# Optimization experiments

Measured on AMD Instinct MI355X. Metric: run time of the kernel, lower is better.

Reference implementation:

```python
import jax, jax.numpy as jnp
import numpy as np

B, S, D = 1, 1024, 2048          # batch, seq, hidden
H, KH, HD = 16, 16, 128          # heads, kv heads, head_dim
E, K, FI = 8, 4, 1408            # experts, top_k, moe_intermediate
FS = 5632                        # shared expert intermediate
WIN = 512                        # sliding window
THETA = 1.0e6                    # rope base
EPS = 1e-6                       # rmsnorm eps


def setup_inputs() -> dict:
    key = jax.random.key(0)
    ks = jax.random.split(key, 16)
    nrm = lambda k, shape: jax.random.normal(k, shape, jnp.float32) * 0.02
    return dict(
        hidden_states=jax.random.normal(ks[0], (B, S, D), jnp.float32),
        ln1_w=jnp.ones((D,), jnp.float32),
        ln2_w=jnp.ones((D,), jnp.float32),
        wq=nrm(ks[1], (D, H * HD)), bq=jnp.zeros((H * HD,), jnp.float32),
        wk=nrm(ks[2], (D, KH * HD)), bk=jnp.zeros((KH * HD,), jnp.float32),
        wv=nrm(ks[3], (D, KH * HD)), bv=jnp.zeros((KH * HD,), jnp.float32),
        wo=nrm(ks[4], (H * HD, D)),
        w_router=nrm(ks[5], (D, E)),
        w_gate_e=nrm(ks[6], (E, D, FI)),
        w_up_e=nrm(ks[7], (E, D, FI)),
        w_down_e=nrm(ks[8], (E, FI, D)),
        ws_gate=nrm(ks[9], (D, FS)),
        ws_up=nrm(ks[10], (D, FS)),
        ws_down=nrm(ks[11], (FS, D)),
        w_shared_gate=nrm(ks[12], (D, 1)),
    )


def _rms(h, w):
    v = jnp.mean(h * h, axis=-1, keepdims=True)
    return h * jax.lax.rsqrt(v + EPS) * w


def _rope(q, k):
    pos = jnp.arange(S, dtype=jnp.float32)
    inv = 1.0 / (THETA ** (jnp.arange(0, HD, 2, dtype=jnp.float32) / HD))
    ang = pos[:, None] * inv[None, :]                      # [S, HD/2]
    cos = jnp.concatenate([jnp.cos(ang)] * 2, -1)[None, :, None, :]
    sin = jnp.concatenate([jnp.sin(ang)] * 2, -1)[None, :, None, :]
    rot = lambda t: jnp.concatenate([-t[..., HD // 2:], t[..., :HD // 2]], -1)
    return q * cos + rot(q) * sin, k * cos + rot(k) * sin


def reference(hidden_states, ln1_w, ln2_w, wq, bq, wk, bk, wv, bv, wo,
              w_router, w_gate_e, w_up_e, w_down_e,
              ws_gate, ws_up, ws_down, w_shared_gate):
    x = hidden_states
    # --- sliding-window causal attention ---
    h = _rms(x, ln1_w)
    q = (h @ wq + bq).reshape(B, S, H, HD)
    k = (h @ wk + bk).reshape(B, S, KH, HD)
    v = (h @ wv + bv).reshape(B, S, KH, HD)
    q, k = _rope(q, k)
    scores = jnp.einsum('bqhd,bkhd->bhqk', q, k) * (HD ** -0.5)
    i = jnp.arange(S)[:, None]
    j = jnp.arange(S)[None, :]
    mask = (j <= i) & (i - j < WIN)                        # causal + window
    scores = jnp.where(mask[None, None], scores, jnp.finfo(scores.dtype).min)
    attn = jax.nn.softmax(scores, axis=-1)
    o = jnp.einsum('bhqk,bkhd->bqhd', attn, v).reshape(B, S, H * HD) @ wo
    x = x + o
    # --- sparse MoE block ---
    h = _rms(x, ln2_w)
    t = h.reshape(B * S, D)
    logits = (t @ w_router).astype(jnp.float32)
    probs = jax.nn.softmax(logits, axis=-1)                # [T, E]
    top_w, top_i = jax.lax.top_k(probs, K)                 # norm_topk_prob=False
    cw = jnp.zeros((B * S, E), probs.dtype).at[jnp.arange(B * S)[:, None], top_i].set(top_w)
    # routed experts (dense combine == gather/dispatch/grouped-GEMM/combine)
    g = jnp.einsum('td,edf->etf', t, w_gate_e)
    u = jnp.einsum('td,edf->etf', t, w_up_e)
    eo = jnp.einsum('etf,efd->etd', jax.nn.silu(g) * u, w_down_e)
    routed = jnp.einsum('te,etd->td', cw, eo)
    # shared expert with sigmoid gate
    shared = (jax.nn.silu(t @ ws_gate) * (t @ ws_up)) @ ws_down
    sgate = jax.nn.sigmoid(t @ w_shared_gate)              # [T, 1]
    moe = routed + sgate * shared
    return x + moe.reshape(B, S, D)
```

## Files before the change

### kernel.cpp

```cpp
#include <hip/hip_runtime.h>

#define S_ 1024
#define D_ 2048
#define H_ 16
#define HD_ 128
#define E_ 8
#define FI_ 1408
#define FS_ 5632
#define WIN_ 512
#define T_ 1024
#define QKVN 6144

typedef _Float16 f16;
typedef __attribute__((ext_vector_type(8))) _Float16 f16x8;
typedef __attribute__((ext_vector_type(4))) _Float16 f16x4;
typedef __attribute__((ext_vector_type(4))) float f32x4;

#define MFMA16(a, b, c) __builtin_amdgcn_mfma_f32_16x16x32_f16((a), (b), (c), 0, 0, 0)

__device__ __forceinline__ void gload16(const void* g, void* l) {
    __builtin_amdgcn_global_load_lds(
        (const __attribute__((address_space(1))) unsigned*)g,
        (__attribute__((address_space(3))) unsigned*)l, 16, 0, 0);
}

__global__ __launch_bounds__(256) void rmsnorm16_kernel(const float* __restrict__ x,
                                                        const float* __restrict__ w,
                                                        f16* __restrict__ out) {
    int t = blockIdx.x;
    const float* xr = x + (long)t * D_;
    int base = threadIdx.x * 8;
    float4 v0 = *(const float4*)(xr + base);
    float4 v1 = *(const float4*)(xr + base + 4);
    float ss = v0.x*v0.x + v0.y*v0.y + v0.z*v0.z + v0.w*v0.w
             + v1.x*v1.x + v1.y*v1.y + v1.z*v1.z + v1.w*v1.w;
    #pragma unroll
    for (int off = 1; off < 64; off <<= 1) ss += __shfl_xor(ss, off);
    __shared__ float red[4];
    if ((threadIdx.x & 63) == 0) red[threadIdx.x >> 6] = ss;
    __syncthreads();
    float tot = red[0] + red[1] + red[2] + red[3];
    float scale = rsqrtf(tot / (float)D_ + 1e-6f);
    float4 w0 = *(const float4*)(w + base);
    float4 w1 = *(const float4*)(w + base + 4);
    f16x8 o;
    o[0] = (f16)(v0.x*scale*w0.x); o[1] = (f16)(v0.y*scale*w0.y);
    o[2] = (f16)(v0.z*scale*w0.z); o[3] = (f16)(v0.w*scale*w0.w);
    o[4] = (f16)(v1.x*scale*w1.x); o[5] = (f16)(v1.y*scale*w1.y);
    o[6] = (f16)(v1.z*scale*w1.z); o[7] = (f16)(v1.w*scale*w1.w);
    *(f16x8*)(out + (long)t * D_ + base) = o;
}

__device__ __forceinline__ void tconv_body(const float* __restrict__ src,
                                           f16* __restrict__ dst,
                                           int K, int N, int mode) {
    int n0 = blockIdx.x * 64, k0 = blockIdx.y * 64;
    __shared__ f16 tile[64][72];
    int t = threadIdx.x, r = t >> 2, c4 = (t & 3) * 16;
    const float* sp = src + (long)(k0 + r) * N + n0 + c4;
    #pragma unroll
    for (int i = 0; i < 16; i += 4) {
        float4 v = *(const float4*)(sp + i);
        tile[c4 + i + 0][r] = (f16)v.x;
        tile[c4 + i + 1][r] = (f16)v.y;
        tile[c4 + i + 2][r] = (f16)v.z;
        tile[c4 + i + 3][r] = (f16)v.w;
    }
    __syncthreads();
    #pragma unroll
    for (int h = 0; h < 2; h++) {
        int v = t + h * 256;
        int nl = v >> 3, c8 = (v & 7) * 8;
        f16x8 vec = *(const f16x8*)&tile[nl][c8];
        int nr = n0 + nl;
        long orow = (mode == 0) ? nr
                  : ((long)(nr >> 4) * 32 + (nr & 15) + (mode == 2 ? 16 : 0));
        *(f16x8*)(dst + orow * K + k0 + c8) = vec;
    }
}

__global__ __launch_bounds__(256) void tconv_kernel(const float* __restrict__ src,
                                                    f16* __restrict__ dst,
                                                    int K, int N, long sSrc, long sDst) {
    tconv_body(src + (long)blockIdx.z * sSrc, dst + (long)blockIdx.z * sDst, K, N, 0);
}

__global__ __launch_bounds__(256) void tconv_gu_kernel(const float* __restrict__ srcA,
                                                       const float* __restrict__ srcB,
                                                       f16* __restrict__ dst,
                                                       int K, int N, long sSrc, long sDst,
                                                       int zsplit) {
    int z = blockIdx.z;
    int e = (z < zsplit) ? z : z - zsplit;
    const float* src = ((z < zsplit) ? srcA : srcB) + (long)e * sSrc;
    tconv_body(src, dst + (long)e * sDst, K, N, (z < zsplit) ? 1 : 2);
}

template <int EPI, int MODE>
__global__ __launch_bounds__(256) void gemm16_kernel(
    const f16* __restrict__ Ag, const f16* __restrict__ BTg,
    void* Cg, const void* auxg,
    const int* __restrict__ tokidx, const int* __restrict__ cntv,
    const float* __restrict__ tw,
    int M, int N, int K, int lda, int ldb,
    long sA, long sB, long sC) {
    int z = blockIdx.z;
    const f16* A = Ag + (long)z * sA;
    const f16* BT = BTg + (long)z * sB;
    int bm = blockIdx.y * 128, bn = blockIdx.x * 128;
    int cnt = M;
    if (MODE >= 1) {
        cnt = cntv[z];
        if (bm >= cnt) return;
    }
    int tid = threadIdx.x, lane = tid & 63, wave = tid >> 6;
    int wm = (wave >> 1) * 64, wn = (wave & 1) * 64;

    __shared__ f16 As[128][64];
    __shared__ f16 Bs[128][64];

    f32x4 acc[4][4];
    #pragma unroll
    for (int i = 0; i < 4; i++)
        #pragma unroll
        for (int j = 0; j < 4; j++) acc[i][j] = (f32x4){0.f, 0.f, 0.f, 0.f};

    int srow8 = lane >> 3;
    int scol = ((lane & 7) ^ srow8) * 8;
    const f16* Abp[4];
    const f16* Bbp[4];
    #pragma unroll
    for (int i = 0; i < 4; i++) {
        int ra = bm + wave * 32 + i * 8 + srow8;
        long arow;
        if (MODE == 1) {
            int tok = (ra < cnt) ? tokidx[z * T_ + ra] : 0;
            arow = tok;
        } else {
            arow = ra;
        }
        Abp[i] = A + arow * (long)lda + scol;
        Bbp[i] = BT + (long)(bn + wave * 32 + i * 8 + srow8) * ldb + scol;
    }

    for (int k0 = 0; k0 < K; k0 += 64) {
        __syncthreads();
        #pragma unroll
        for (int i = 0; i < 4; i++) {
            gload16(Abp[i] + k0, &As[wave * 32 + i * 8][0]);
            gload16(Bbp[i] + k0, &Bs[wave * 32 + i * 8][0]);
        }
        __syncthreads();
        #pragma unroll
        for (int kk = 0; kk < 64; kk += 32) {
            f16x8 af[4], bf[4];
            #pragma unroll
            for (int mi = 0; mi < 4; mi++) {
                int r = wm + mi * 16 + (lane & 15);
                int c = ((kk >> 3) + (lane >> 4)) ^ (r & 7);
                af[mi] = *(const f16x8*)((const char*)&As[r][0] + (c << 4));
            }
            #pragma unroll
            for (int ni = 0; ni < 4; ni++) {
                int r = wn + ni * 16 + (lane & 15);
                int c = ((kk >> 3) + (lane >> 4)) ^ (r & 7);
                bf[ni] = *(const f16x8*)((const char*)&Bs[r][0] + (c << 4));
            }
            #pragma unroll
            for (int mi = 0; mi < 4; mi++)
                #pragma unroll
                for (int ni = 0; ni < 4; ni++)
                    acc[mi][ni] = MFMA16(af[mi], bf[ni], acc[mi][ni]);
        }
    }

    if (EPI == 5) {
        int half = N >> 1;
        #pragma unroll
        for (int mi = 0; mi < 4; mi++) {
            #pragma unroll
            for (int p = 0; p < 2; p++) {
                #pragma unroll
                for (int i = 0; i < 4; i++) {
                    int m = bm + wm + mi * 16 + (lane >> 4) * 4 + i;
                    int j = ((bn + wn) >> 1) + p * 16 + (lane & 15);
                    float g = acc[mi][2 * p][i];
                    float u = acc[mi][2 * p + 1][i];
                    ((f16*)Cg + (long)z * sC)[(long)m * half + j] =
                        (f16)(g / (1.f + __expf(-g)) * u);
                }
            }
        }
        return;
    }
    #pragma unroll
    for (int mi = 0; mi < 4; mi++) {
        #pragma unroll
        for (int ni = 0; ni < 4; ni++) {
            #pragma unroll
            for (int i = 0; i < 4; i++) {
                int m = bm + wm + mi * 16 + (lane >> 4) * 4 + i;
                int n = bn + wn + ni * 16 + (lane & 15);
                long idx = (long)m * N + n;
                float v = acc[mi][ni][i];
                if (EPI == 1) {
                    ((f16*)Cg)[idx] = (f16)(v + ((const float*)auxg)[n]);
                } else if (EPI == 4) {
                    ((float*)Cg + (long)z * sC)[idx] = v;
                } else if (EPI == 6) {
                    float wv = tw[z * T_ + m];
                    ((f16*)Cg + (long)z * sC)[idx] = (f16)(v * wv);
                }
            }
        }
    }
}

__global__ __launch_bounds__(256) void rope16_kernel(f16* __restrict__ qkv) {
    int s = blockIdx.x;
    float fs = (float)s;
    for (int p = threadIdx.x; p < H_ * 64; p += 256) {
        int h = p >> 6, j = p & 63;
        float inv = __expf(-(float)j * (13.815510557964274f / 64.f));
        float ang = fs * inv;
        float c = cosf(ang), sn = sinf(ang);
        long base = (long)s * QKVN + h * HD_ + j;
        float q1 = (float)qkv[base], q2 = (float)qkv[base + 64];
        qkv[base] = (f16)(q1 * c - q2 * sn);
        qkv[base + 64] = (f16)(q2 * c + q1 * sn);
        long kb = base + 2048;
        float k1 = (float)qkv[kb], k2 = (float)qkv[kb + 64];
        qkv[kb] = (f16)(k1 * c - k2 * sn);
        qkv[kb + 64] = (f16)(k2 * c + k1 * sn);
    }
}

__global__ __launch_bounds__(256) void attn16_kernel(const f16* __restrict__ qkv,
                                                     f16* __restrict__ Og) {
    int qt = blockIdx.x * 64;
    int head = blockIdx.y;
    int tid = threadIdx.x, lane = tid & 63, wave = tid >> 6;

    __shared__ f16 Ks[64][128];
    __shared__ f16 Vrow[64][128];
    __shared__ f16 VsT[128][64];
    __shared__ f16 Ps[4][16][64];

    int qr = qt + wave * 16 + (lane & 15);
    const f16* Qp = qkv + (long)qr * QKVN + head * HD_;
    f16x8 qf[4];
    #pragma unroll
    for (int kk = 0; kk < 4; kk++)
        qf[kk] = *(const f16x8*)(Qp + kk * 32 + (lane >> 4) * 8);

    f32x4 oacc[8];
    #pragma unroll
    for (int db = 0; db < 8; db++) oacc[db] = (f32x4){0.f, 0.f, 0.f, 0.f};
    float m_run[4] = {-1e30f, -1e30f, -1e30f, -1e30f};
    float l_run[4] = {0.f, 0.f, 0.f, 0.f};

    int k_lo = qt - (WIN_ - 1);
    if (k_lo < 0) k_lo = 0;
    k_lo &= ~63;

    for (int k0 = k_lo; k0 < qt + 64; k0 += 64) {
        __syncthreads();
        {
            int row = tid >> 2, cq = (tid & 3) * 32;
            const f16* Kp = qkv + (long)(k0 + row) * QKVN + 2048 + head * HD_ + cq;
            const f16* Vp = Kp + 2048;
            #pragma unroll
            for (int u = 0; u < 32; u += 8) {
                f16x8 tk = *(const f16x8*)(Kp + u);
                int co = ((cq + u) * 2) ^ ((row & 7) << 4);
                *(f16x8*)((char*)&Ks[row][0] + co) = tk;
                *(f16x8*)(&Vrow[row][cq + u]) = *(const f16x8*)(Vp + u);
            }
        }
        __syncthreads();
        {
            int d = tid >> 1, ks = (tid & 1) * 32;
            f16 tmp[32];
            #pragma unroll
            for (int j = 0; j < 32; j++) tmp[j] = Vrow[ks + j][d];
            #pragma unroll
            for (int u = 0; u < 32; u += 8) {
                int co = ((ks + u) * 2) ^ ((d & 7) << 4);
                f16x8 tv;
                #pragma unroll
                for (int j = 0; j < 8; j++) tv[j] = tmp[u + j];
                *(f16x8*)((char*)&VsT[d][0] + co) = tv;
            }
        }
        f32x4 sacc[4];
        #pragma unroll
        for (int cb = 0; cb < 4; cb++) sacc[cb] = (f32x4){0.f, 0.f, 0.f, 0.f};
        #pragma unroll
        for (int kk = 0; kk < 4; kk++) {
            #pragma unroll
            for (int cb = 0; cb < 4; cb++) {
                int krow = cb * 16 + (lane & 15);
                int co = ((kk * 32 + (lane >> 4) * 8) * 2) ^ ((krow & 7) << 4);
                f16x8 kf = *(const f16x8*)((const char*)&Ks[krow][0] + co);
                sacc[cb] = MFMA16(qf[kk], kf, sacc[cb]);
            }
        }
        float mtile[4] = {-1e30f, -1e30f, -1e30f, -1e30f};
        #pragma unroll
        for (int cb = 0; cb < 4; cb++) {
            #pragma unroll
            for (int i = 0; i < 4; i++) {
                int qi = qt + wave * 16 + (lane >> 4) * 4 + i;
                int kj = k0 + cb * 16 + (lane & 15);
                float s = sacc[cb][i] * 0.08838834764831845f;
                bool valid = (kj <= qi) && (qi - kj < WIN_);
                s = valid ? s : -1e30f;
                sacc[cb][i] = s;
                mtile[i] = fmaxf(mtile[i], s);
            }
        }
        #pragma unroll
        for (int i = 0; i < 4; i++) {
            float v = mtile[i];
            v = fmaxf(v, __shfl_xor(v, 1));
            v = fmaxf(v, __shfl_xor(v, 2));
            v = fmaxf(v, __shfl_xor(v, 4));
            v = fmaxf(v, __shfl_xor(v, 8));
            mtile[i] = v;
        }
        float pscale[4], lsum[4];
        #pragma unroll
        for (int i = 0; i < 4; i++) {
            float mnew = fmaxf(m_run[i], mtile[i]);
            pscale[i] = __expf(m_run[i] - mnew);
            m_run[i] = mnew;
            lsum[i] = 0.f;
        }
        #pragma unroll
        for (int cb = 0; cb < 4; cb++) {
            #pragma unroll
            for (int i = 0; i < 4; i++) {
                float mn = fmaxf(m_run[i], -1e20f);
                float p = __expf(sacc[cb][i] - mn);
                lsum[i] += p;
                int prow = (lane >> 4) * 4 + i;
                int pcol = cb * 16 + (lane & 15);
                int co = (pcol * 2) ^ ((prow & 7) << 4);
                *(f16*)((char*)&Ps[wave][prow][0] + co) = (f16)p;
            }
        }
        #pragma unroll
        for (int i = 0; i < 4; i++) {
            float v = lsum[i];
            v += __shfl_xor(v, 1);
            v += __shfl_xor(v, 2);
            v += __shfl_xor(v, 4);
            v += __shfl_xor(v, 8);
            l_run[i] = l_run[i] * pscale[i] + v;
        }
        #pragma unroll
        for (int db = 0; db < 8; db++)
            #pragma unroll
            for (int i = 0; i < 4; i++) oacc[db][i] *= pscale[i];
        __syncthreads();
        #pragma unroll
        for (int ks = 0; ks < 2; ks++) {
            int prow = lane & 15;
            int co = ((ks * 32 + (lane >> 4) * 8) * 2) ^ ((prow & 7) << 4);
            f16x8 pf = *(const f16x8*)((const char*)&Ps[wave][prow][0] + co);
            #pragma unroll
            for (int db = 0; db < 8; db++) {
                int vrow2 = db * 16 + (lane & 15);
                int co2 = ((ks * 32 + (lane >> 4) * 8) * 2) ^ ((vrow2 & 7) << 4);
                f16x8 vf = *(const f16x8*)((const char*)&VsT[vrow2][0] + co2);
                oacc[db] = MFMA16(pf, vf, oacc[db]);
            }
        }
    }
    #pragma unroll
    for (int db = 0; db < 8; db++) {
        #pragma unroll
        for (int i = 0; i < 4; i++) {
            int qi = qt + wave * 16 + (lane >> 4) * 4 + i;
            int d = db * 16 + (lane & 15);
            Og[(long)qi * D_ + head * HD_ + d] = (f16)(oacc[db][i] / l_run[i]);
        }
    }
}

__global__ __launch_bounds__(256) void postattn_kernel(
    const float* __restrict__ x, const float* __restrict__ p,
    const float* __restrict__ ln2, const float* __restrict__ wr,
    const float* __restrict__ wshg,
    float* __restrict__ x2, f16* __restrict__ h2,
    float* __restrict__ cw, float* __restrict__ sgate) {
    int t = blockIdx.x;
    int base = threadIdx.x * 8;
    long ro = (long)t * D_ + base;
    const long plane = (long)T_ * D_;
    float xv[8];
    #pragma unroll
    for (int j = 0; j < 8; j += 4) {
        float4 a = *(const float4*)(x + ro + j);
        float4 b = *(const float4*)(p + ro + j);
        float4 c = *(const float4*)(p + plane + ro + j);
        xv[j + 0] = a.x + b.x + c.x;
        xv[j + 1] = a.y + b.y + c.y;
        xv[j + 2] = a.z + b.z + c.z;
        xv[j + 3] = a.w + b.w + c.w;
    }
    *(float4*)(x2 + ro) = *(float4*)&xv[0];
    *(float4*)(x2 + ro + 4) = *(float4*)&xv[4];

    float ss = 0.f;
    #pragma unroll
    for (int j = 0; j < 8; j++) ss += xv[j] * xv[j];
    #pragma unroll
    for (int off = 1; off < 64; off <<= 1) ss += __shfl_xor(ss, off);
    __shared__ float red0[4];
    if ((threadIdx.x & 63) == 0) red0[threadIdx.x >> 6] = ss;
    __syncthreads();
    float scale = rsqrtf((red0[0] + red0[1] + red0[2] + red0[3]) / (float)D_ + 1e-6f);

    float part[9] = {0.f,0.f,0.f,0.f,0.f,0.f,0.f,0.f,0.f};
    f16x8 ho;
    #pragma unroll
    for (int j = 0; j < 8; j++) {
        int d = base + j;
        float hv = xv[j] * scale * ln2[d];
        ho[j] = (f16)hv;
        const float* wrow = wr + (long)d * E_;
        #pragma unroll
        for (int e = 0; e < 8; e++) part[e] += hv * wrow[e];
        part[8] += hv * wshg[d];
    }
    *(f16x8*)(h2 + ro) = ho;

    #pragma unroll
    for (int e = 0; e < 9; e++) {
        float v = part[e];
        #pragma unroll
        for (int off = 1; off < 64; off <<= 1) v += __shfl_xor(v, off);
        part[e] = v;
    }
    __shared__ float red[4][9];
    int lane = threadIdx.x & 63, wave = threadIdx.x >> 6;
    if (lane == 0)
        #pragma unroll
        for (int e = 0; e < 9; e++) red[wave][e] = part[e];
    __syncthreads();
    if (threadIdx.x == 0) {
        float logit[9];
        #pragma unroll
        for (int e = 0; e < 9; e++) logit[e] = red[0][e] + red[1][e] + red[2][e] + red[3][e];
        float mx = logit[0];
        #pragma unroll
        for (int e = 1; e < 8; e++) mx = fmaxf(mx, logit[e]);
        float pp[8], sum = 0.f;
        #pragma unroll
        for (int e = 0; e < 8; e++) { pp[e] = expf(logit[e] - mx); sum += pp[e]; }
        #pragma unroll
        for (int e = 0; e < 8; e++) pp[e] /= sum;
        float sel[8] = {0.f,0.f,0.f,0.f,0.f,0.f,0.f,0.f};
        float tmp[8];
        #pragma unroll
        for (int e = 0; e < 8; e++) tmp[e] = pp[e];
        for (int it = 0; it < 4; it++) {
            int best = 0;
            float bvv = tmp[0];
            #pragma unroll
            for (int e = 1; e < 8; e++)
                if (tmp[e] > bvv) { bvv = tmp[e]; best = e; }
            sel[best] = pp[best];
            tmp[best] = -1.f;
        }
        #pragma unroll
        for (int e = 0; e < 8; e++) cw[(long)e * T_ + t] = sel[e];
        sgate[t] = 1.f / (1.f + expf(-logit[8]));
    }
}

__global__ __launch_bounds__(512) void bucket_kernel(const float* __restrict__ cw,
                                                     int* __restrict__ cnt,
                                                     int* __restrict__ tokidx,
                                                     float* __restrict__ tw,
                                                     int* __restrict__ posmat) {
    int e = threadIdx.x >> 6, lane = threadIdx.x & 63;
    int count = 0;
    for (int base = 0; base < T_; base += 64) {
        int t = base + lane;
        float wv = cw[(long)e * T_ + t];
        unsigned long long m = __ballot(wv > 0.f);
        int pre = __popcll(m & ((1ull << lane) - 1ull));
        if (wv > 0.f) {
            int s = count + pre;
            tokidx[e * T_ + s] = t;
            tw[e * T_ + s] = wv;
            posmat[e * T_ + t] = s;
        }
        count += __popcll(m);
    }
    if (lane == 0) cnt[e] = count;
}

__global__ __launch_bounds__(256) void biascat_kernel(const float* bq, const float* bk,
                                                      const float* bv, float* bqkv) {
    int i = blockIdx.x * 256 + threadIdx.x;
    if (i < 2048) bqkv[i] = bq[i];
    else if (i < 4096) bqkv[i] = bk[i - 2048];
    else if (i < 6144) bqkv[i] = bv[i - 4096];
}

__global__ __launch_bounds__(256) void reduce4_kernel(const float* __restrict__ p,
                                                      float* __restrict__ out) {
    long total = (long)T_ * D_ / 4;
    for (long i = (long)blockIdx.x * 256 + threadIdx.x; i < total;
         i += (long)gridDim.x * 256) {
        float4 a = ((const float4*)p)[i];
        float4 b = ((const float4*)p)[i + total];
        float4 c = ((const float4*)p)[i + 2 * total];
        float4 d = ((const float4*)p)[i + 3 * total];
        float4 o;
        o.x = a.x + b.x + c.x + d.x; o.y = a.y + b.y + c.y + d.y;
        o.z = a.z + b.z + c.z + d.z; o.w = a.w + b.w + c.w + d.w;
        ((float4*)out)[i] = o;
    }
}

__global__ __launch_bounds__(256) void combine_kernel(
    const float* __restrict__ x2, const float* __restrict__ sho,
    const float* __restrict__ sg, const float* __restrict__ cw,
    const int* __restrict__ posmat, const f16* __restrict__ eo,
    float* __restrict__ out) {
    long total = (long)T_ * D_ / 4;
    for (long i = (long)blockIdx.x * 256 + threadIdx.x; i < total;
         i += (long)gridDim.x * 256) {
        int t = (int)(i >> 9);
        int c4 = (int)(i & 511) * 4;
        float4 a = ((const float4*)x2)[i];
        float4 s = ((const float4*)sho)[i];
        float g = sg[t];
        float r0 = a.x + g * s.x, r1 = a.y + g * s.y;
        float r2 = a.z + g * s.z, r3 = a.w + g * s.w;
        #pragma unroll
        for (int e = 0; e < 8; e++) {
            float w = cw[(long)e * T_ + t];
            if (w > 0.f) {
                int slot = posmat[(long)e * T_ + t];
                f16x4 v = *(const f16x4*)(eo + ((long)e * T_ + slot) * D_ + c4);
                r0 += (float)v[0]; r1 += (float)v[1];
                r2 += (float)v[2]; r3 += (float)v[3];
            }
        }
        float4 o; o.x = r0; o.y = r1; o.z = r2; o.w = r3;
        ((float4*)out)[i] = o;
    }
}

extern "C" void kernel_launch(void* const* d_in, const int* in_sizes, int n_in,
                              void* d_out, int out_size, void* d_ws, size_t ws_size,
                              hipStream_t stream) {
    const float* x    = (const float*)d_in[0];
    const float* ln1  = (const float*)d_in[1];
    const float* ln2  = (const float*)d_in[2];
    const float* wq   = (const float*)d_in[3];
    const float* bq   = (const float*)d_in[4];
    const float* wk   = (const float*)d_in[5];
    const float* bk   = (const float*)d_in[6];
    const float* wv   = (const float*)d_in[7];
    const float* bv   = (const float*)d_in[8];
    const float* wo   = (const float*)d_in[9];
    const float* wrt  = (const float*)d_in[10];
    const float* wge  = (const float*)d_in[11];
    const float* wue  = (const float*)d_in[12];
    const float* wde  = (const float*)d_in[13];
    const float* wsg  = (const float*)d_in[14];
    const float* wsu  = (const float*)d_in[15];
    const float* wsd  = (const float*)d_in[16];
    const float* wshg = (const float*)d_in[17];

    float* ws = (float*)d_ws;
    f16*   wT     = (f16*)ws;
    float* x2     = ws + 11534336;
    float* sho    = x2 + 2097152;
    float* bqkv   = sho + 2097152;
    float* cw     = bqkv + 6144;
    float* sg     = cw + 8192;
    int*   cnt    = (int*)(sg + 1024);
    int*   tokidx = cnt + 8;
    float* tw     = (float*)(tokidx + 8192);
    int*   posmat = (int*)(tw + 8192);
    f16*   h1     = (f16*)(posmat + 8192);
    f16*   h2     = (f16*)((float*)h1 + 1048576);
    float* pool   = (float*)h2 + 1048576;

    f16*   qkv     = (f16*)pool;
    float* woparts = pool + 3145728;
    f16*   sgb     = (f16*)pool;
    float* parts4  = pool + 2883584;
    f16*   Gg      = (f16*)pool;
    f16*   eo      = (f16*)(pool + 5767168);
    f16*   ao      = h1;

    dim3 blk(256);

    rmsnorm16_kernel<<<T_, blk, 0, stream>>>(x, ln1, h1);
    biascat_kernel<<<24, blk, 0, stream>>>(bq, bk, bv, bqkv);
    tconv_kernel<<<dim3(32, 32, 1), blk, 0, stream>>>(wq, wT, 2048, 2048, 0, 0);
    tconv_kernel<<<dim3(32, 32, 1), blk, 0, stream>>>(wk, wT + 2048L * 2048, 2048, 2048, 0, 0);
    tconv_kernel<<<dim3(32, 32, 1), blk, 0, stream>>>(wv, wT + 4096L * 2048, 2048, 2048, 0, 0);
    gemm16_kernel<1, 0><<<dim3(48, 8, 1), blk, 0, stream>>>(
        h1, wT, qkv, bqkv, nullptr, nullptr, nullptr,
        T_, QKVN, D_, 2048, 2048, 0, 0, 0);
    rope16_kernel<<<S_, blk, 0, stream>>>(qkv);
    attn16_kernel<<<dim3(16, 16), blk, 0, stream>>>(qkv, ao);
    tconv_kernel<<<dim3(32, 32, 1), blk, 0, stream>>>(wo, wT, 2048, 2048, 0, 0);
    gemm16_kernel<4, 0><<<dim3(16, 8, 2), blk, 0, stream>>>(
        ao, wT, woparts, nullptr, nullptr, nullptr, nullptr,
        T_, D_, 1024, 2048, 2048, 1024, 1024, 2097152);
    postattn_kernel<<<T_, blk, 0, stream>>>(x, woparts, ln2, wrt, wshg, x2, h2, cw, sg);
    bucket_kernel<<<1, 512, 0, stream>>>(cw, cnt, tokidx, tw, posmat);

    tconv_gu_kernel<<<dim3(88, 32, 2), blk, 0, stream>>>(wsg, wsu, wT, 2048, 5632, 0, 0, 1);
    gemm16_kernel<5, 0><<<dim3(88, 8, 1), blk, 0, stream>>>(
        h2, wT, sgb, nullptr, nullptr, nullptr, nullptr,
        T_, 2 * FS_, D_, 2048, 2048, 0, 0, 0);
    tconv_kernel<<<dim3(32, 88, 1), blk, 0, stream>>>(wsd, wT, 5632, 2048, 0, 0);
    gemm16_kernel<4, 0><<<dim3(16, 8, 4), blk, 0, stream>>>(
        sgb, wT, parts4, nullptr, nullptr, nullptr, nullptr,
        T_, D_, 1408, 5632, 5632, 1408, 1408, 2097152);
    reduce4_kernel<<<512, blk, 0, stream>>>(parts4, sho);

    tconv_gu_kernel<<<dim3(22, 32, 8), blk, 0, stream>>>(
        wge, wue, wT, 2048, 1408, 2048L * 1408, 2816L * 2048, 4);
    gemm16_kernel<5, 1><<<dim3(22, 8, 4), blk, 0, stream>>>(
        h2, wT, Gg, nullptr, tokidx, cnt, nullptr,
        T_, 2 * FI_, D_, 2048, 2048, 0, 2816L * 2048, 1024L * 1408);
    tconv_gu_kernel<<<dim3(22, 32, 8), blk, 0, stream>>>(
        wge + 4L * 2048 * 1408, wue + 4L * 2048 * 1408, wT, 2048, 1408,
        2048L * 1408, 2816L * 2048, 4);
    gemm16_kernel<5, 1><<<dim3(22, 8, 4), blk, 0, stream>>>(
        h2, wT, Gg + 4L * 1024 * 1408, nullptr, tokidx + 4 * T_, cnt + 4, nullptr,
        T_, 2 * FI_, D_, 2048, 2048, 0, 2816L * 2048, 1024L * 1408);

    tconv_kernel<<<dim3(32, 22, 4), blk, 0, stream>>>(wde, wT, 1408, 2048,
                                                      1408L * 2048, 2048L * 1408);
    gemm16_kernel<6, 2><<<dim3(16, 8, 4), blk, 0, stream>>>(
        Gg, wT, eo, nullptr, nullptr, cnt, tw,
        T_, D_, 1408, 1408, 1408, 1024L * 1408, 2048L * 1408, 1024L * 2048);
    tconv_kernel<<<dim3(32, 22, 4), blk, 0, stream>>>(wde + 4L * 1408 * 2048, wT, 1408, 2048,
                                                      1408L * 2048, 2048L * 1408);
    gemm16_kernel<6, 2><<<dim3(16, 8, 4), blk, 0, stream>>>(
        Gg + 4L * 1024 * 1408, wT, eo + 4L * 1024 * 2048, nullptr, nullptr, cnt + 4, tw + 4 * T_,
        T_, D_, 1408, 1408, 1408, 1024L * 1408, 2048L * 1408, 1024L * 2048);

    combine_kernel<<<1024, blk, 0, stream>>>(x2, sho, sg, cw, posmat, eo, (float*)d_out);
}
```

Measured before the change: 578.4 us.

## Batch weight conversions, remap GEMM block order, raise MFMA priority in attention

Merges the four Q/K/V/O weight conversions into one launch, and the two down-projection conversion+GEMM halves into single launches covering all eight experts. This cuts launch count and tail effects. The GEMM block index is remapped across groups of 8 in a strided pattern, likely to spread neighbouring tiles across XCDs or improve L2 locality. The attention MFMA sections are wrapped in s_setprio to favour matrix-issuing waves. The merged down-projection needs enough workspace for all eight experts' transposed weights at once, which increases the memory footprint.

```diff
diff --git a/kernel.cpp b/kernel.cpp
--- a/kernel.cpp
+++ b/kernel.cpp
@@ -85,6 +85,16 @@
     tconv_body(src + (long)blockIdx.z * sSrc, dst + (long)blockIdx.z * sDst, K, N, 0);
 }
 
+__global__ __launch_bounds__(256) void tconv_qkvo_kernel(const float* __restrict__ wq,
+                                                         const float* __restrict__ wk,
+                                                         const float* __restrict__ wv,
+                                                         const float* __restrict__ wo,
+                                                         f16* __restrict__ dst) {
+    int z = blockIdx.z;
+    const float* src = (z == 0) ? wq : (z == 1) ? wk : (z == 2) ? wv : wo;
+    tconv_body(src, dst + (long)z * 2048 * 2048, 2048, 2048, 0);
+}
+
 __global__ __launch_bounds__(256) void tconv_gu_kernel(const float* __restrict__ srcA,
                                                        const float* __restrict__ srcB,
                                                        f16* __restrict__ dst,
@@ -107,7 +117,13 @@
     int z = blockIdx.z;
     const f16* A = Ag + (long)z * sA;
     const f16* BT = BTg + (long)z * sB;
-    int bm = blockIdx.y * 128, bn = blockIdx.x * 128;
+
+    int nxy = gridDim.x * gridDim.y;
+    int pid = blockIdx.y * gridDim.x + blockIdx.x;
+    if ((nxy & 7) == 0) pid = (pid & 7) * (nxy >> 3) + (pid >> 3);
+    int bx = pid / gridDim.y, by = pid % gridDim.y;
+    int bm = by * 128, bn = bx * 128;
+
     int cnt = M;
     if (MODE >= 1) {
         cnt = cntv[z];
@@ -295,6 +311,7 @@
         f32x4 sacc[4];
         #pragma unroll
         for (int cb = 0; cb < 4; cb++) sacc[cb] = (f32x4){0.f, 0.f, 0.f, 0.f};
+        __builtin_amdgcn_s_setprio(1);
         #pragma unroll
         for (int kk = 0; kk < 4; kk++) {
             #pragma unroll
@@ -305,6 +322,7 @@
                 sacc[cb] = MFMA16(qf[kk], kf, sacc[cb]);
             }
         }
+        __builtin_amdgcn_s_setprio(0);
         float mtile[4] = {-1e30f, -1e30f, -1e30f, -1e30f};
         #pragma unroll
         for (int cb = 0; cb < 4; cb++) {
@@ -363,6 +381,7 @@
             #pragma unroll
             for (int i = 0; i < 4; i++) oacc[db][i] *= pscale[i];
         __syncthreads();
+        __builtin_amdgcn_s_setprio(1);
         #pragma unroll
         for (int ks = 0; ks < 2; ks++) {
             int prow = lane & 15;
@@ -376,6 +395,7 @@
                 oacc[db] = MFMA16(pf, vf, oacc[db]);
             }
         }
+        __builtin_amdgcn_s_setprio(0);
     }
     #pragma unroll
     for (int db = 0; db < 8; db++) {
@@ -606,17 +626,14 @@
 
     rmsnorm16_kernel<<<T_, blk, 0, stream>>>(x, ln1, h1);
     biascat_kernel<<<24, blk, 0, stream>>>(bq, bk, bv, bqkv);
-    tconv_kernel<<<dim3(32, 32, 1), blk, 0, stream>>>(wq, wT, 2048, 2048, 0, 0);
-    tconv_kernel<<<dim3(32, 32, 1), blk, 0, stream>>>(wk, wT + 2048L * 2048, 2048, 2048, 0, 0);
-    tconv_kernel<<<dim3(32, 32, 1), blk, 0, stream>>>(wv, wT + 4096L * 2048, 2048, 2048, 0, 0);
+    tconv_qkvo_kernel<<<dim3(32, 32, 4), blk, 0, stream>>>(wq, wk, wv, wo, wT);
     gemm16_kernel<1, 0><<<dim3(48, 8, 1), blk, 0, stream>>>(
         h1, wT, qkv, bqkv, nullptr, nullptr, nullptr,
         T_, QKVN, D_, 2048, 2048, 0, 0, 0);
     rope16_kernel<<<S_, blk, 0, stream>>>(qkv);
     attn16_kernel<<<dim3(16, 16), blk, 0, stream>>>(qkv, ao);
-    tconv_kernel<<<dim3(32, 32, 1), blk, 0, stream>>>(wo, wT, 2048, 2048, 0, 0);
     gemm16_kernel<4, 0><<<dim3(16, 8, 2), blk, 0, stream>>>(
-        ao, wT, woparts, nullptr, nullptr, nullptr, nullptr,
+        ao, wT + 6144L * 2048, woparts, nullptr, nullptr, nullptr, nullptr,
         T_, D_, 1024, 2048, 2048, 1024, 1024, 2097152);
     postattn_kernel<<<T_, blk, 0, stream>>>(x, woparts, ln2, wrt, wshg, x2, h2, cw, sg);
     bucket_kernel<<<1, 512, 0, stream>>>(cw, cnt, tokidx, tw, posmat);
@@ -643,16 +660,11 @@
         h2, wT, Gg + 4L * 1024 * 1408, nullptr, tokidx + 4 * T_, cnt + 4, nullptr,
         T_, 2 * FI_, D_, 2048, 2048, 0, 2816L * 2048, 1024L * 1408);
 
-    tconv_kernel<<<dim3(32, 22, 4), blk, 0, stream>>>(wde, wT, 1408, 2048,
+    tconv_kernel<<<dim3(32, 22, 8), blk, 0, stream>>>(wde, wT, 1408, 2048,
                                                       1408L * 2048, 2048L * 1408);
-    gemm16_kernel<6, 2><<<dim3(16, 8, 4), blk, 0, stream>>>(
+    gemm16_kernel<6, 2><<<dim3(16, 8, 8), blk, 0, stream>>>(
         Gg, wT, eo, nullptr, nullptr, cnt, tw,
         T_, D_, 1408, 1408, 1408, 1024L * 1408, 2048L * 1408, 1024L * 2048);
-    tconv_kernel<<<dim3(32, 22, 4), blk, 0, stream>>>(wde + 4L * 1408 * 2048, wT, 1408, 2048,
-                                                      1408L * 2048, 2048L * 1408);
-    gemm16_kernel<6, 2><<<dim3(16, 8, 4), blk, 0, stream>>>(
-        Gg + 4L * 1024 * 1408, wT, eo + 4L * 1024 * 2048, nullptr, nullptr, cnt + 4, tw + 4 * T_,
-        T_, D_, 1408, 1408, 1408, 1024L * 1408, 2048L * 1408, 1024L * 2048);
 
     combine_kernel<<<1024, blk, 0, stream>>>(x2, sho, sg, cw, posmat, eo, (float*)d_out);
 }
```

Measured after the change: 555.2 us. 1.04x faster.
